# Kernel tuning notes

Hardware: AMD Instinct MI355X
Metric: run time of the kernel (lower is better)

The kernel has to match this reference:

```python
import jax
import jax.numpy as jnp
from jax import lax
import numpy as np

B, C, H, W = 16, 96, 112, 112
HIDDEN = 4 * C
LN_EPS = 1e-6  # ConvNeXt LayerNorm eps


def setup_inputs() -> dict:
    key = jax.random.key(0)
    ks = jax.random.split(key, 8)
    x = jax.random.normal(ks[0], (B, C, H, W), dtype=jnp.float32)
    # depthwise 7x7 kernel, HWIO with feature_group_count=C -> (7,7,1,C)
    dw_w = jax.random.normal(ks[1], (7, 7, 1, C), dtype=jnp.float32) * 0.02
    dw_b = jnp.zeros((C,), dtype=jnp.float32)
    gamma = jnp.ones((C,), dtype=jnp.float32)
    beta = jnp.zeros((C,), dtype=jnp.float32)
    w1 = jax.random.normal(ks[2], (C, HIDDEN), dtype=jnp.float32) * 0.02
    b1 = jnp.zeros((HIDDEN,), dtype=jnp.float32)
    w2 = jax.random.normal(ks[3], (HIDDEN, C), dtype=jnp.float32) * 0.02
    b2 = jnp.zeros((C,), dtype=jnp.float32)
    scale = jnp.full((C,), 1e-6, dtype=jnp.float32)  # block_scale init 1e-6
    return {"x": x, "dw_w": dw_w, "dw_b": dw_b, "gamma": gamma, "beta": beta,
            "w1": w1, "b1": b1, "w2": w2, "b2": b2, "scale": scale}


def reference(x, dw_w, dw_b, gamma, beta, w1, b1, w2, b2, scale):
    # depthwise 7x7, stride 1, padding 3 (SAME), groups = C
    y = lax.conv_general_dilated(
        x, dw_w, window_strides=(1, 1), padding="SAME",
        dimension_numbers=("NCHW", "HWIO", "NCHW"),
        feature_group_count=C,
    ) + dw_b[None, :, None, None]
    # BCHW -> BHWC
    y = jnp.transpose(y, (0, 2, 3, 1))
    # LayerNorm over channel dim
    mu = jnp.mean(y, axis=-1, keepdims=True)
    var = jnp.var(y, axis=-1, keepdims=True)
    y = (y - mu) * lax.rsqrt(var + LN_EPS) * gamma + beta
    # pointwise MLP with exact GELU (torch nn.GELU default)
    h = jax.nn.gelu(jnp.einsum("bhwc,cd->bhwd", y, w1) + b1, approximate=False)
    y = jnp.einsum("bhwd,dc->bhwc", h, w2) + b2
    # BHWC -> BCHW, scale, residual (eval mode: stochastic depth = identity)
    y = jnp.transpose(y, (0, 3, 1, 2))
    return scale[None, :, None, None] * y + x
```

## Files before the change

### kernel.cpp

```cpp
#include <hip/hip_runtime.h>
#include <hip/hip_bf16.h>

#define BATCH 16
#define CCH 96
#define HH 112
#define WW 112
#define HID 384
#define NPIX (BATCH * HH * WW)
#define HW (HH * WW)

#define PXB 128
#define ZROWD 50
#define SLICE_B 12288
#define RING_SLOTS 3
#define ZR_BYTES (PXB * ZROWD * 4)
#define B1_OFF (RING_SLOTS * SLICE_B)
#define SMEM_TOTAL (B1_OFF + 1536)

#define XSTR 132

typedef __attribute__((ext_vector_type(8))) short bf16x8;
typedef __attribute__((ext_vector_type(4))) float f32x4;
typedef __attribute__((ext_vector_type(4))) unsigned int uint4v;

typedef const __attribute__((address_space(1))) void gvoid_t;
typedef __attribute__((address_space(3))) void svoid_t;

__device__ __forceinline__ short f2bf(float v) {
    __hip_bfloat16 h = __float2bfloat16(v);
    return __builtin_bit_cast(short, h);
}
__device__ __forceinline__ float bf2f(short s) {
    unsigned int u = ((unsigned int)(unsigned short)s) << 16;
    return __builtin_bit_cast(float, u);
}
__device__ __forceinline__ float gelu_fast(float v) {
    float e = __expf(-1.702f * v);
    return v * __builtin_amdgcn_rcpf(1.0f + e);
}

__global__ __launch_bounds__(256) void pack_w(const float* __restrict__ w1,
                                              const float* __restrict__ w2,
                                              const float* __restrict__ gamma,
                                              const float* __restrict__ scale,
                                              short* __restrict__ wp) {
    int o = blockIdx.x * 256 + threadIdx.x;
    if (o >= 12 * 12 * 64 * 8) return;
    const int j   = o & 7;
    const int l   = (o >> 3) & 63;
    const int g   = o >> 9;
    const int f   = g % 12;
    const int kk2 = g / 12;
    float v;
    if (f < 6) {
        const int kk = f >> 1, mh = f & 1;
        const int c  = kk * 32 + (l >> 4) * 8 + j;
        const int d  = (2 * kk2 + mh) * 16 + (l & 15);
        v = gamma[c] * w1[c * HID + d];
    } else {
        const int nt2 = f - 6;
        const int dd  = kk2 * 32 + ((j >> 2) << 4) + ((l >> 4) << 2) + (j & 3);
        const int n   = nt2 * 16 + (l & 15);
        v = w2[dd * CCH + n] * scale[n];
    }
    wp[o] = f2bf(v);
}

__global__ __launch_bounds__(256) void pack_bias(const float* __restrict__ w1,
                                                 const float* __restrict__ b1,
                                                 const float* __restrict__ beta,
                                                 const float* __restrict__ b2,
                                                 const float* __restrict__ scale,
                                                 float* __restrict__ b1p,
                                                 float* __restrict__ b2p) {
    int t = blockIdx.x * 256 + threadIdx.x;
    if (t < HID) {
        float s = b1[t];
        for (int c = 0; c < CCH; ++c) s += beta[c] * w1[c * HID + t];
        b1p[t] = s;
    } else if (t < HID + CCH) {
        int c = t - HID;
        b2p[c] = scale[c] * b2[c];
    }
}

__global__ __launch_bounds__(256) void conv_kernel(
    const float* __restrict__ x, const float* __restrict__ dww,
    const float* __restrict__ dwb, short* __restrict__ y)
{
    __shared__ float xs[34 * XSTR];

    const int t = threadIdx.x;
    const int p = blockIdx.x;
    int o = (p & 7) * 768 + (p >> 3);
    const int ht = o & 3;  o >>= 2;
    const int c  = o % CCH;
    const int b  = o / CCH;
    const int h0 = ht * 28;
    const float* xc = x + (size_t)(b * CCH + c) * HW;

    float4 vbuf[5];
    #pragma unroll
    for (int k = 0; k < 5; ++k) {
        const int idx = t + 256 * k;
        const int r  = idx >> 5;
        const int j  = idx & 31;
        const int gh = h0 - 3 + r;
        float4 v = make_float4(0.f, 0.f, 0.f, 0.f);
        if (idx < 1088 && (unsigned)gh < HH && j >= 1 && j <= 28)
            v = *reinterpret_cast<const float4*>(xc + gh * WW + 4 * j - 4);
        vbuf[k] = v;
    }
    #pragma unroll
    for (int k = 0; k < 5; ++k) {
        const int idx = t + 256 * k;
        if (idx < 1088)
            *reinterpret_cast<float4*>(&xs[(idx >> 5) * XSTR + (idx & 31) * 4]) = vbuf[k];
    }
    __syncthreads();

    const int wg = t >> 5;
    const int r  = t & 31;
    if (wg < 7 && r < 28) {
        const int j0 = wg * 16;
        const float bias = dwb[c];
        float acc[16];
        #pragma unroll
        for (int i = 0; i < 16; ++i) acc[i] = bias;
        #pragma unroll
        for (int kh = 0; kh < 7; ++kh) {
            f32x4 qd[6];
            #pragma unroll
            for (int u = 0; u < 6; ++u)
                qd[u] = *reinterpret_cast<const f32x4*>(&xs[(r + kh) * XSTR + j0 + 4 * u]);
            #pragma unroll
            for (int kw = 0; kw < 7; ++kw) {
                const float wt = dww[(kh * 7 + kw) * CCH + c];
                #pragma unroll
                for (int i = 0; i < 16; ++i) {
                    const int jj = i + kw + 1;
                    acc[i] += qd[jj >> 2][jj & 3] * wt;
                }
            }
        }
        uint4v w0, w1v;
        #pragma unroll
        for (int u = 0; u < 4; ++u) {
            w0[u]  = (unsigned int)(unsigned short)f2bf(acc[2 * u]) |
                     ((unsigned int)(unsigned short)f2bf(acc[2 * u + 1]) << 16);
            w1v[u] = (unsigned int)(unsigned short)f2bf(acc[8 + 2 * u]) |
                     ((unsigned int)(unsigned short)f2bf(acc[9 + 2 * u]) << 16);
        }
        short* yc = y + (size_t)(b * CCH + c) * HW + (h0 + r) * WW + j0;
        *reinterpret_cast<uint4v*>(yc)     = w0;
        *reinterpret_cast<uint4v*>(yc + 8) = w1v;
    }
}

__global__ __launch_bounds__(256, 4) void mlp_kernel(
    const short* __restrict__ ybuf, const char* __restrict__ wp,
    const float* __restrict__ b1p, const float* __restrict__ b2p,
    const float* __restrict__ x, float* __restrict__ out)
{
    __shared__ __align__(16) char smem[SMEM_TOTAL];
    unsigned int* zr = (unsigned int*)smem;
    float* b1l = (float*)(smem + B1_OFF);

    const int t    = threadIdx.x;
    const int lane = t & 63;
    const int wv   = t >> 6;
    const int l15  = lane & 15;
    const int q    = lane >> 4;
    const int px0  = blockIdx.x * PXB;
    const int b    = px0 / HW;
    const int hw0  = px0 - b * HW;

    if (t < 192) {
        const int pq = t / 48;
        const int cp = t - pq * 48;
        const unsigned int* Ap = (const unsigned int*)(ybuf +
            (size_t)(b * CCH + 2 * cp) * HW + hw0 + pq * 32);
        const unsigned int* Bp = (const unsigned int*)(ybuf +
            (size_t)(b * CCH + 2 * cp + 1) * HW + hw0 + pq * 32);
        #pragma unroll
        for (int e = 0; e < 4; ++e) {
            const uint4v A  = *reinterpret_cast<const uint4v*>(Ap + e * 4);
            const uint4v Bv = *reinterpret_cast<const uint4v*>(Bp + e * 4);
            #pragma unroll
            for (int k = 0; k < 4; ++k) {
                const int px = pq * 32 + e * 8 + 2 * k;
                zr[px * ZROWD + cp]       = (A[k] & 0xffffu) | (Bv[k] << 16);
                zr[(px + 1) * ZROWD + cp] = (A[k] >> 16) | (Bv[k] & 0xffff0000u);
            }
        }
    } else {
        const int i0 = (t - 192) * 6;
        #pragma unroll
        for (int i2 = 0; i2 < 6; ++i2) b1l[i0 + i2] = b1p[i0 + i2];
    }

    f32x4 acc2[2][6];
    #pragma unroll
    for (int nt2 = 0; nt2 < 6; ++nt2) {
        const int c = nt2 * 16 + l15;
        const float bv = b2p[c];
        #pragma unroll
        for (int m2 = 0; m2 < 2; ++m2) {
            const size_t g = (size_t)(b * CCH + c) * HW + hw0 + wv * 32 + m2 * 16 + q * 4;
            const f32x4 xv = *reinterpret_cast<const f32x4*>(x + g);
            acc2[m2][nt2].x = bv + xv.x;  acc2[m2][nt2].y = bv + xv.y;
            acc2[m2][nt2].z = bv + xv.z;  acc2[m2][nt2].w = bv + xv.w;
        }
    }
    __syncthreads();

    bf16x8 za[2][3];
    #pragma unroll
    for (int nt = 0; nt < 2; ++nt) {
        const int row = wv * 32 + nt * 16 + l15;
        const char* base = smem + row * (ZROWD * 4) + q * 16;
        float s1 = 0.f, s2 = 0.f;
        #pragma unroll
        for (int kk = 0; kk < 3; ++kk) {
            za[nt][kk] = *reinterpret_cast<const bf16x8*>(base + kk * 64);
            #pragma unroll
            for (int j = 0; j < 8; ++j) {
                const float v = bf2f(za[nt][kk][j]);
                s1 += v; s2 += v * v;
            }
        }
        s1 += __shfl_xor(s1, 16, 64);  s2 += __shfl_xor(s2, 16, 64);
        s1 += __shfl_xor(s1, 32, 64);  s2 += __shfl_xor(s2, 32, 64);
        const float mu   = s1 * (1.0f / CCH);
        const float rstd = rsqrtf(s2 * (1.0f / CCH) - mu * mu + 1e-6f);
        #pragma unroll
        for (int kk = 0; kk < 3; ++kk)
            #pragma unroll
            for (int j = 0; j < 8; ++j)
                za[nt][kk][j] = f2bf((bf2f(za[nt][kk][j]) - mu) * rstd);
    }
    __syncthreads();

    asm volatile("s_waitcnt vmcnt(0)" ::: "memory");

    #define STAGE_F(SL, SLOT)                                                       \
        {                                                                           \
            const char* _s = wp + (size_t)(SL) * SLICE_B + (wv * 3) * 1024 +        \
                             lane * 16;                                             \
            char* _d = smem + (SLOT) * SLICE_B + (wv * 3) * 1024;                   \
            __builtin_amdgcn_global_load_lds((gvoid_t*)(_s),        (svoid_t*)(_d),        16, 0, 0); \
            __builtin_amdgcn_global_load_lds((gvoid_t*)(_s + 1024), (svoid_t*)(_d + 1024), 16, 0, 0); \
            __builtin_amdgcn_global_load_lds((gvoid_t*)(_s + 2048), (svoid_t*)(_d + 2048), 16, 0, 0); \
        }
    #define WAITBAR()                                                               \
        {                                                                           \
            asm volatile("s_waitcnt vmcnt(3)" ::: "memory");                        \
            __builtin_amdgcn_s_barrier();                                           \
            __builtin_amdgcn_sched_barrier(0);                                      \
        }

    STAGE_F(0, 0);

    #pragma unroll
    for (int kk2 = 0; kk2 < 12; ++kk2) {
        {
            const int sl = (kk2 + 1 > 11) ? 11 : kk2 + 1;
            STAGE_F(sl, sl % RING_SLOTS);
        }
        WAITBAR();
        const char* wb = smem + (kk2 % RING_SLOTS) * SLICE_B + lane * 16;

        f32x4 p0[2], p1[2];
        const f32x4 bva = *reinterpret_cast<const f32x4*>(b1l + 32 * kk2 + q * 4);
        const f32x4 bvb = *reinterpret_cast<const f32x4*>(b1l + 32 * kk2 + 16 + q * 4);
        p0[0] = bva;  p0[1] = bva;
        p1[0] = bvb;  p1[1] = bvb;
        #pragma unroll
        for (int kk = 0; kk < 3; ++kk) {
            const bf16x8 wfa = *reinterpret_cast<const bf16x8*>(wb + (kk * 2) * 1024);
            const bf16x8 wfb = *reinterpret_cast<const bf16x8*>(wb + (kk * 2 + 1) * 1024);
            p0[0] = __builtin_amdgcn_mfma_f32_16x16x32_bf16(wfa, za[0][kk], p0[0], 0, 0, 0);
            p0[1] = __builtin_amdgcn_mfma_f32_16x16x32_bf16(wfa, za[1][kk], p0[1], 0, 0, 0);
            p1[0] = __builtin_amdgcn_mfma_f32_16x16x32_bf16(wfb, za[0][kk], p1[0], 0, 0, 0);
            p1[1] = __builtin_amdgcn_mfma_f32_16x16x32_bf16(wfb, za[1][kk], p1[1], 0, 0, 0);
        }
        bf16x8 hv[2];
        #pragma unroll
        for (int nt = 0; nt < 2; ++nt)
            #pragma unroll
            for (int i = 0; i < 4; ++i) {
                hv[nt][i]     = f2bf(gelu_fast(p0[nt][i]));
                hv[nt][4 + i] = f2bf(gelu_fast(p1[nt][i]));
            }
        #pragma unroll
        for (int nt2 = 0; nt2 < 6; ++nt2) {
            const bf16x8 bfr = *reinterpret_cast<const bf16x8*>(wb + (6 + nt2) * 1024);
            acc2[0][nt2] = __builtin_amdgcn_mfma_f32_16x16x32_bf16(hv[0], bfr, acc2[0][nt2], 0, 0, 0);
            acc2[1][nt2] = __builtin_amdgcn_mfma_f32_16x16x32_bf16(hv[1], bfr, acc2[1][nt2], 0, 0, 0);
        }
    }
    #undef STAGE_F
    #undef WAITBAR

    #pragma unroll
    for (int m2 = 0; m2 < 2; ++m2) {
        const int pxl = hw0 + wv * 32 + m2 * 16 + q * 4;
        #pragma unroll
        for (int nt2 = 0; nt2 < 6; ++nt2) {
            const int c = nt2 * 16 + l15;
            const size_t g = (size_t)(b * CCH + c) * HW + pxl;
            *reinterpret_cast<f32x4*>(out + g) = acc2[m2][nt2];
        }
    }
}

extern "C" void kernel_launch(void* const* d_in, const int* in_sizes, int n_in,
                              void* d_out, int out_size, void* d_ws, size_t ws_size,
                              hipStream_t stream) {
    const float* x     = (const float*)d_in[0];
    const float* dww   = (const float*)d_in[1];
    const float* dwb   = (const float*)d_in[2];
    const float* gamma = (const float*)d_in[3];
    const float* beta  = (const float*)d_in[4];
    const float* w1    = (const float*)d_in[5];
    const float* b1    = (const float*)d_in[6];
    const float* w2    = (const float*)d_in[7];
    const float* b2    = (const float*)d_in[8];
    const float* scale = (const float*)d_in[9];
    float* out = (float*)d_out;

    char* ws = (char*)d_ws;
    short* ybuf = (short*)ws;
    const size_t Y_BYTES = (size_t)NPIX * CCH * 2;
    short* wp  = (short*)(ws + Y_BYTES);
    float* b1p = (float*)(ws + Y_BYTES + 12 * SLICE_B);
    float* b2p = b1p + HID;

    pack_w<<<(12 * 12 * 64 * 8 + 255) / 256, 256, 0, stream>>>(w1, w2, gamma, scale, wp);
    pack_bias<<<2, 256, 0, stream>>>(w1, b1, beta, b2, scale, b1p, b2p);
    conv_kernel<<<BATCH * CCH * 4, 256, 0, stream>>>(x, dww, dwb, ybuf);
    mlp_kernel<<<NPIX / PXB, 256, 0, stream>>>(ybuf, (const char*)wp, b1p, b2p, x, out);
}
```

Measured before the change: 119.2 us.

## Compute two output rows per thread in depthwise conv to reuse LDS loads

Each conv block now covers half an image plane (56 rows) instead of a quarter, and each thread computes two adjacent output rows. The 8 input rows it reads from LDS feed both accumulators, so LDS reads per output drop and the halo overhead per block shrinks. In exchange each thread holds 32 accumulators instead of 16, which raises register pressure, and the grid is half as large.

After: 112.4 us, median of 2. 1.06x faster.

```diff
diff --git a/kernel.cpp b/kernel.cpp
--- a/kernel.cpp
+++ b/kernel.cpp
@@ -18,6 +18,7 @@
 #define SMEM_TOTAL (B1_OFF + 1536)
 
 #define XSTR 132
+#define CXROWS 62
 
 typedef __attribute__((ext_vector_type(8))) short bf16x8;
 typedef __attribute__((ext_vector_type(4))) float f32x4;
@@ -88,72 +89,89 @@
     const float* __restrict__ x, const float* __restrict__ dww,
     const float* __restrict__ dwb, short* __restrict__ y)
 {
-    __shared__ float xs[34 * XSTR];
+    __shared__ float xs[CXROWS * XSTR];
 
     const int t = threadIdx.x;
     const int p = blockIdx.x;
-    int o = (p & 7) * 768 + (p >> 3);
-    const int ht = o & 3;  o >>= 2;
+    int o = (p & 7) * 384 + (p >> 3);
+    const int hh = o & 1;  o >>= 1;
     const int c  = o % CCH;
     const int b  = o / CCH;
-    const int h0 = ht * 28;
+    const int h0 = hh * 56;
     const float* xc = x + (size_t)(b * CCH + c) * HW;
 
-    float4 vbuf[5];
-    #pragma unroll
-    for (int k = 0; k < 5; ++k) {
+    float4 vbuf[8];
+    #pragma unroll
+    for (int k = 0; k < 8; ++k) {
         const int idx = t + 256 * k;
         const int r  = idx >> 5;
         const int j  = idx & 31;
         const int gh = h0 - 3 + r;
         float4 v = make_float4(0.f, 0.f, 0.f, 0.f);
-        if (idx < 1088 && (unsigned)gh < HH && j >= 1 && j <= 28)
+        if (idx < CXROWS * 32 && (unsigned)gh < HH && j >= 1 && j <= 28)
             v = *reinterpret_cast<const float4*>(xc + gh * WW + 4 * j - 4);
         vbuf[k] = v;
     }
     #pragma unroll
-    for (int k = 0; k < 5; ++k) {
+    for (int k = 0; k < 8; ++k) {
         const int idx = t + 256 * k;
-        if (idx < 1088)
+        if (idx < CXROWS * 32)
             *reinterpret_cast<float4*>(&xs[(idx >> 5) * XSTR + (idx & 31) * 4]) = vbuf[k];
     }
     __syncthreads();
 
-    const int wg = t >> 5;
-    const int r  = t & 31;
-    if (wg < 7 && r < 28) {
-        const int j0 = wg * 16;
+    const int cg = t >> 5;
+    const int rg = t & 31;
+    if (cg < 7 && rg < 28) {
+        const int r0 = rg * 2;
+        const int j0 = cg * 16;
         const float bias = dwb[c];
-        float acc[16];
-        #pragma unroll
-        for (int i = 0; i < 16; ++i) acc[i] = bias;
-        #pragma unroll
-        for (int kh = 0; kh < 7; ++kh) {
+        float acc0[16], acc1[16];
+        #pragma unroll
+        for (int i = 0; i < 16; ++i) { acc0[i] = bias; acc1[i] = bias; }
+        #pragma unroll
+        for (int ir = 0; ir < 8; ++ir) {
             f32x4 qd[6];
             #pragma unroll
             for (int u = 0; u < 6; ++u)
-                qd[u] = *reinterpret_cast<const f32x4*>(&xs[(r + kh) * XSTR + j0 + 4 * u]);
+                qd[u] = *reinterpret_cast<const f32x4*>(&xs[(r0 + ir) * XSTR + j0 + 4 * u]);
             #pragma unroll
             for (int kw = 0; kw < 7; ++kw) {
-                const float wt = dww[(kh * 7 + kw) * CCH + c];
-                #pragma unroll
-                for (int i = 0; i < 16; ++i) {
-                    const int jj = i + kw + 1;
-                    acc[i] += qd[jj >> 2][jj & 3] * wt;
+                if (ir <= 6) {
+                    const float wt = dww[(ir * 7 + kw) * CCH + c];
+                    #pragma unroll
+                    for (int i = 0; i < 16; ++i) {
+                        const int jj = i + kw + 1;
+                        acc0[i] += qd[jj >> 2][jj & 3] * wt;
+                    }
+                }
+                if (ir >= 1) {
+                    const float wt = dww[((ir - 1) * 7 + kw) * CCH + c];
+                    #pragma unroll
+                    for (int i = 0; i < 16; ++i) {
+                        const int jj = i + kw + 1;
+                        acc1[i] += qd[jj >> 2][jj & 3] * wt;
+                    }
                 }
             }
         }
-        uint4v w0, w1v;
+        uint4v wa, wb2, wc, wd;
         #pragma unroll
         for (int u = 0; u < 4; ++u) {
-            w0[u]  = (unsigned int)(unsigned short)f2bf(acc[2 * u]) |
-                     ((unsigned int)(unsigned short)f2bf(acc[2 * u + 1]) << 16);
-            w1v[u] = (unsigned int)(unsigned short)f2bf(acc[8 + 2 * u]) |
-                     ((unsigned int)(unsigned short)f2bf(acc[9 + 2 * u]) << 16);
-        }
-        short* yc = y + (size_t)(b * CCH + c) * HW + (h0 + r) * WW + j0;
-        *reinterpret_cast<uint4v*>(yc)     = w0;
-        *reinterpret_cast<uint4v*>(yc + 8) = w1v;
+            wa[u] = (unsigned int)(unsigned short)f2bf(acc0[2 * u]) |
+                    ((unsigned int)(unsigned short)f2bf(acc0[2 * u + 1]) << 16);
+            wb2[u] = (unsigned int)(unsigned short)f2bf(acc0[8 + 2 * u]) |
+                    ((unsigned int)(unsigned short)f2bf(acc0[9 + 2 * u]) << 16);
+            wc[u] = (unsigned int)(unsigned short)f2bf(acc1[2 * u]) |
+                    ((unsigned int)(unsigned short)f2bf(acc1[2 * u + 1]) << 16);
+            wd[u] = (unsigned int)(unsigned short)f2bf(acc1[8 + 2 * u]) |
+                    ((unsigned int)(unsigned short)f2bf(acc1[9 + 2 * u]) << 16);
+        }
+        short* yc = y + (size_t)(b * CCH + c) * HW + (h0 + r0) * WW + j0;
+        *reinterpret_cast<uint4v*>(yc)          = wa;
+        *reinterpret_cast<uint4v*>(yc + 8)      = wb2;
+        *reinterpret_cast<uint4v*>(yc + WW)     = wc;
+        *reinterpret_cast<uint4v*>(yc + WW + 8) = wd;
     }
 }
 
@@ -338,6 +356,6 @@
 
     pack_w<<<(12 * 12 * 64 * 8 + 255) / 256, 256, 0, stream>>>(w1, w2, gamma, scale, wp);
     pack_bias<<<2, 256, 0, stream>>>(w1, b1, beta, b2, scale, b1p, b2p);
-    conv_kernel<<<BATCH * CCH * 4, 256, 0, stream>>>(x, dww, dwb, ybuf);
+    conv_kernel<<<BATCH * CCH * 2, 256, 0, stream>>>(x, dww, dwb, ybuf);
     mlp_kernel<<<NPIX / PXB, 256, 0, stream>>>(ybuf, (const char*)wp, b1p, b2p, x, out);
 }
```
